# Kernel optimization log

Measured on AMD Instinct MI355X. Metric: run time of the kernel, lower is better.

## Reference

```python
import jax, jax.numpy as jnp
import numpy as np

N = 50000
E = 1_600_000
N_INP = 128
N_HID = 128
N_OUT = 64
N_LAYERS = 2


def setup_inputs() -> dict:
    key = jax.random.key(0)
    ks = jax.random.split(key, 12)
    s = 1.0 / np.sqrt(N_HID)
    return {
        "node_attr": jax.random.normal(ks[0], (N, N_INP), dtype=jnp.float32),
        "edge_index": jax.random.randint(ks[1], (2, E), 0, N, dtype=jnp.int64),
        "batch_idx": jnp.zeros((N,), dtype=jnp.int64),
        "adv_atts": jax.random.uniform(ks[2], (N_LAYERS, E), dtype=jnp.float32, minval=0.05, maxval=1.0),
        "W_inp": jax.random.normal(ks[3], (N_HID, N_INP), dtype=jnp.float32) * (1.0 / np.sqrt(N_INP)),
        "b_inp": jnp.zeros((N_HID,), dtype=jnp.float32),
        "W_a": jax.random.normal(ks[4], (N_LAYERS, N_HID, N_HID), dtype=jnp.float32) * s,
        "b_a": jnp.zeros((N_LAYERS, N_HID), dtype=jnp.float32),
        "ln_w": jnp.ones((N_LAYERS, N_HID), dtype=jnp.float32),
        "ln_b": jnp.zeros((N_LAYERS, N_HID), dtype=jnp.float32),
        "W_out": jax.random.normal(ks[5], (N_OUT, N_HID), dtype=jnp.float32) * s,
        "b_out": jnp.zeros((N_OUT,), dtype=jnp.float32),
    }


def _layer_norm(x, w, b, eps=1e-5):
    mu = jnp.mean(x, axis=-1, keepdims=True)
    var = jnp.mean(jnp.square(x - mu), axis=-1, keepdims=True)
    return (x - mu) * jax.lax.rsqrt(var + eps) * w + b


def _segment_softmax(logits, seg, num_segments):
    # PyG softmax: numerically-stable softmax grouped by target node id
    m = jax.ops.segment_max(logits, seg, num_segments=num_segments)
    e = jnp.exp(logits - m[seg])
    s = jax.ops.segment_sum(e, seg, num_segments=num_segments)
    return e / (s[seg] + 1e-16)


def reference(node_attr, edge_index, batch_idx, adv_atts,
              W_inp, b_inp, W_a, b_a, ln_w, ln_b, W_out, b_out):
    src = edge_index[0]  # j (source)
    dst = edge_index[1]  # i (target)
    n = node_attr.shape[0]
    # dropout is identity at inference; initial norm is overwritten (dead code)
    node_rep = node_attr @ W_inp.T + b_inp  # [N, H]
    for l in range(W_a.shape[0]):
        att = _segment_softmax(jnp.log(adv_atts[l]), dst, n)        # [E]
        msg = node_rep[src] * att[:, None]                          # [E, H]
        aggr = jax.ops.segment_sum(msg, dst, num_segments=n)        # [N, H]
        h = (aggr + node_rep) @ W_a[l].T + b_a[l]
        node_rep = _layer_norm(jax.nn.gelu(h, approximate=False), ln_w[l], ln_b[l])
    # node_level == True
    return node_rep @ W_out.T + b_out
```

## Files before the change

### kernel.cpp

```cpp
#include <hip/hip_runtime.h>
#include <hip/hip_bf16.h>
#include <math.h>


#define WAVE 64
#define NPARTS 32
#define CHUNKE 4096
#define CB 64

typedef __attribute__((ext_vector_type(8))) short bf16x8;
typedef __attribute__((ext_vector_type(4))) float f32x4;
union ABu { uint4 u; bf16x8 v; };
union ABh { ushort h[8]; bf16x8 v; };

static __device__ __forceinline__ float bf2f(uint u16) {
    union { uint i; float f; } c;
    c.i = u16 << 16;
    return c.f;
}
static __device__ __forceinline__ uint f2bf(float f) {
    uint x = __float_as_uint(f);
    return (x + 0x7FFFu + ((x >> 16) & 1u)) >> 16;
}

__global__ void k_count(const int* __restrict__ dst, int E,
                        int* __restrict__ deg, int* __restrict__ rank) {
    int e = blockIdx.x * blockDim.x + threadIdx.x;
    if (e < E) rank[e] = atomicAdd(&deg[dst[e]], 1);
}

__global__ __launch_bounds__(256) void k_scan1(const int* __restrict__ deg, int n,
                                               int* __restrict__ excl,
                                               int* __restrict__ bsum) {
    __shared__ int sd[256];
    int t = threadIdx.x, i = blockIdx.x * 256 + t;
    int v = (i < n) ? deg[i] : 0;
    sd[t] = v;
    __syncthreads();
    for (int off = 1; off < 256; off <<= 1) {
        int u = (t >= off) ? sd[t - off] : 0;
        __syncthreads();
        sd[t] += u;
        __syncthreads();
    }
    if (i < n) excl[i] = sd[t] - v;
    if (t == 255) bsum[blockIdx.x] = sd[255];
}

__global__ __launch_bounds__(256) void k_scan2(int* __restrict__ bsum, int nb) {
    __shared__ int sd[256];
    int t = threadIdx.x;
    int v = (t < nb) ? bsum[t] : 0;
    sd[t] = v;
    __syncthreads();
    for (int off = 1; off < 256; off <<= 1) {
        int u = (t >= off) ? sd[t - off] : 0;
        __syncthreads();
        sd[t] += u;
        __syncthreads();
    }
    if (t < nb) bsum[t] = sd[t] - v;
}

__global__ __launch_bounds__(256) void k_scan3(const int* __restrict__ deg,
                                               const int* __restrict__ excl,
                                               const int* __restrict__ bsum, int n,
                                               int* __restrict__ row_ptr) {
    int i = blockIdx.x * 256 + threadIdx.x;
    if (i < n) {
        int rp = bsum[blockIdx.x] + excl[i];
        row_ptr[i] = rp;
        if (i == n - 1) row_ptr[n] = rp + deg[i];
    }
}

__global__ __launch_bounds__(256) void k_bin(const int* __restrict__ src,
                                             const int* __restrict__ dst,
                                             const float* __restrict__ adv,
                                             const int* __restrict__ rank,
                                             const int* __restrict__ row_ptr,
                                             int E, int PART,
                                             int4* __restrict__ tmp,
                                             int* __restrict__ bstart,
                                             int* __restrict__ bcnt) {
    __shared__ int hist[NPARTS], cur[NPARTS], base_[NPARTS];
    __shared__ int4 buf[CHUNKE];
    int c = blockIdx.x;
    int e0 = c * CHUNKE;
    int cnt = min(CHUNKE, E - e0);
    int dreg[CHUNKE / 256];
    int preg[CHUNKE / 256];
    if (threadIdx.x < NPARTS) hist[threadIdx.x] = 0;
    __syncthreads();
#pragma unroll
    for (int i = 0; i < CHUNKE / 256; ++i) {
        int idx = threadIdx.x + i * 256;
        if (idx < cnt) {
            int d = dst[e0 + idx];
            int pt = d / PART;
            dreg[i] = d;
            preg[i] = pt;
            atomicAdd(&hist[pt], 1);
        }
    }
    __syncthreads();
    if (threadIdx.x == 0) {
        int run = 0;
        for (int p = 0; p < NPARTS; ++p) {
            base_[p] = run;
            cur[p] = run;
            run += hist[p];
        }
    }
    __syncthreads();
#pragma unroll
    for (int i = 0; i < CHUNKE / 256; ++i) {
        int idx = threadIdx.x + i * 256;
        if (idx < cnt) {
            int e = e0 + idx;
            int slot = atomicAdd(&cur[preg[i]], 1);
            int pos = row_ptr[dreg[i]] + rank[e];
            buf[slot] = make_int4(src[e], __float_as_int(adv[e]),
                                  __float_as_int(adv[E + e]), pos);
        }
    }
    __syncthreads();
    for (int i = threadIdx.x; i < cnt; i += 256) tmp[(size_t)e0 + i] = buf[i];
    if (threadIdx.x < NPARTS) {
        bstart[c * NPARTS + threadIdx.x] = e0 + base_[threadIdx.x];
        bcnt[c * NPARTS + threadIdx.x] = hist[threadIdx.x];
    }
}

__global__ __launch_bounds__(256) void k_place(const int4* __restrict__ tmp,
                                               const int* __restrict__ bstart,
                                               const int* __restrict__ bcnt,
                                               int nchunk, int4* __restrict__ csr) {
    int xcd = blockIdx.x & 7;
    int j = blockIdx.x >> 3;
    for (int ph = 0; ph < NPARTS / 8; ++ph) {
        int part = xcd + 8 * ph;
        for (int c = j; c < nchunk; c += CB) {
            int s = bstart[c * NPARTS + part];
            int cnt = bcnt[c * NPARTS + part];
            for (int i = threadIdx.x; i < cnt; i += 256) {
                int4 r = tmp[(size_t)s + i];
                csr[r.w] = r;
            }
        }
    }
}

__global__ __launch_bounds__(512) void k_aggr(const uint* __restrict__ rep32,
                                              const int* __restrict__ row_ptr,
                                              const int4* __restrict__ csr, int aoff,
                                              uint* __restrict__ xout, int n) {
    int wave = threadIdx.x >> 6, lane = threadIdx.x & 63;
    int node = blockIdx.x * 8 + wave;
    if (node >= n) return;
    int s0 = row_ptr[node], s1 = row_ptr[node + 1];
    float accx = 0.f, accy = 0.f, ssum = 0.f, amax = 0.f;
    int s = s0;
    for (; s + 8 <= s1; s += 8) {
        int4 c0 = csr[s], c1 = csr[s + 1], c2 = csr[s + 2], c3 = csr[s + 3];
        int4 c4 = csr[s + 4], c5 = csr[s + 5], c6 = csr[s + 6], c7 = csr[s + 7];
        float a0 = __int_as_float(aoff == 1 ? c0.y : c0.z);
        float a1 = __int_as_float(aoff == 1 ? c1.y : c1.z);
        float a2 = __int_as_float(aoff == 1 ? c2.y : c2.z);
        float a3 = __int_as_float(aoff == 1 ? c3.y : c3.z);
        float a4 = __int_as_float(aoff == 1 ? c4.y : c4.z);
        float a5 = __int_as_float(aoff == 1 ? c5.y : c5.z);
        float a6 = __int_as_float(aoff == 1 ? c6.y : c6.z);
        float a7 = __int_as_float(aoff == 1 ? c7.y : c7.z);
        uint r0 = rep32[(size_t)c0.x * 64 + lane];
        uint r1 = rep32[(size_t)c1.x * 64 + lane];
        uint r2 = rep32[(size_t)c2.x * 64 + lane];
        uint r3 = rep32[(size_t)c3.x * 64 + lane];
        uint r4 = rep32[(size_t)c4.x * 64 + lane];
        uint r5 = rep32[(size_t)c5.x * 64 + lane];
        uint r6 = rep32[(size_t)c6.x * 64 + lane];
        uint r7 = rep32[(size_t)c7.x * 64 + lane];
        ssum += a0 + a1 + a2 + a3 + a4 + a5 + a6 + a7;
        amax = fmaxf(amax, fmaxf(fmaxf(fmaxf(a0, a1), fmaxf(a2, a3)),
                                 fmaxf(fmaxf(a4, a5), fmaxf(a6, a7))));
        accx = fmaf(a0, bf2f(r0 & 0xffffu), accx);
        accy = fmaf(a0, bf2f(r0 >> 16), accy);
        accx = fmaf(a1, bf2f(r1 & 0xffffu), accx);
        accy = fmaf(a1, bf2f(r1 >> 16), accy);
        accx = fmaf(a2, bf2f(r2 & 0xffffu), accx);
        accy = fmaf(a2, bf2f(r2 >> 16), accy);
        accx = fmaf(a3, bf2f(r3 & 0xffffu), accx);
        accy = fmaf(a3, bf2f(r3 >> 16), accy);
        accx = fmaf(a4, bf2f(r4 & 0xffffu), accx);
        accy = fmaf(a4, bf2f(r4 >> 16), accy);
        accx = fmaf(a5, bf2f(r5 & 0xffffu), accx);
        accy = fmaf(a5, bf2f(r5 >> 16), accy);
        accx = fmaf(a6, bf2f(r6 & 0xffffu), accx);
        accy = fmaf(a6, bf2f(r6 >> 16), accy);
        accx = fmaf(a7, bf2f(r7 & 0xffffu), accx);
        accy = fmaf(a7, bf2f(r7 >> 16), accy);
    }
    for (; s < s1; ++s) {
        int4 c = csr[s];
        float a = __int_as_float(aoff == 1 ? c.y : c.z);
        uint r = rep32[(size_t)c.x * 64 + lane];
        ssum += a;
        amax = fmaxf(amax, a);
        accx = fmaf(a, bf2f(r & 0xffffu), accx);
        accy = fmaf(a, bf2f(r >> 16), accy);
    }
    float inv = (s1 > s0) ? 1.f / (ssum + amax * 1e-16f) : 0.f;
    uint m = rep32[(size_t)node * 64 + lane];
    float ox = fmaf(accx, inv, bf2f(m & 0xffffu));
    float oy = fmaf(accy, inv, bf2f(m >> 16));
    xout[(size_t)node * 64 + lane] = f2bf(ox) | (f2bf(oy) << 16);
}

#define WROW 136

__global__ __launch_bounds__(512) void k_mlp(const uint* __restrict__ x32,
                                             const float* __restrict__ W,
                                             const float* __restrict__ b,
                                             const float* __restrict__ lw,
                                             const float* __restrict__ lb,
                                             uint* __restrict__ out32, int n) {
    __shared__ ushort Wbf[128 * WROW];
    uint* wd = (uint*)Wbf;
    for (int idx = threadIdx.x; idx < 128 * 64; idx += 512) {
        int row = idx >> 6, d = idx & 63;
        float2 w2 = *(const float2*)&W[row * 128 + d * 2];
        wd[row * (WROW / 2) + d] = f2bf(w2.x) | (f2bf(w2.y) << 16);
    }
    __syncthreads();
    int wv = threadIdx.x >> 6, l = threadIdx.x & 63;
    int c = l & 15, q = l >> 4;
    int base = blockIdx.x * 256 + wv * 32;
    int r0 = min(base + c, n - 1);
    int r1 = min(base + 16 + c, n - 1);

    f32x4 acc[2][8];
#pragma unroll
    for (int rt = 0; rt < 2; ++rt)
#pragma unroll
        for (int ct = 0; ct < 8; ++ct) acc[rt][ct] = (f32x4){0.f, 0.f, 0.f, 0.f};

#pragma unroll
    for (int kb = 0; kb < 4; ++kb) {
        ABu a0, a1;
        a0.u = *(const uint4*)&x32[(size_t)r0 * 64 + kb * 16 + q * 4];
        a1.u = *(const uint4*)&x32[(size_t)r1 * 64 + kb * 16 + q * 4];
#pragma unroll
        for (int ct = 0; ct < 8; ++ct) {
            bf16x8 bf = *(const bf16x8*)&Wbf[(ct * 16 + c) * WROW + kb * 32 + q * 8];
            acc[0][ct] = __builtin_amdgcn_mfma_f32_16x16x32_bf16(a0.v, bf, acc[0][ct], 0, 0, 0);
            acc[1][ct] = __builtin_amdgcn_mfma_f32_16x16x32_bf16(a1.v, bf, acc[1][ct], 0, 0, 0);
        }
    }

    float bias[8], lwv[8], lbv[8];
#pragma unroll
    for (int ct = 0; ct < 8; ++ct) {
        bias[ct] = b[ct * 16 + c];
        lwv[ct] = lw[ct * 16 + c];
        lbv[ct] = lb[ct * 16 + c];
    }

#pragma unroll
    for (int rt = 0; rt < 2; ++rt) {
#pragma unroll
        for (int ct = 0; ct < 8; ++ct)
#pragma unroll
            for (int i = 0; i < 4; ++i) {
                float h = acc[rt][ct][i] + bias[ct];
                acc[rt][ct][i] = 0.5f * h * (1.f + erff(h * 0.70710678118654752f));
            }
        float mu[4], rstd[4];
#pragma unroll
        for (int i = 0; i < 4; ++i) {
            float s = 0.f;
#pragma unroll
            for (int ct = 0; ct < 8; ++ct) s += acc[rt][ct][i];
            s += __shfl_xor(s, 1);
            s += __shfl_xor(s, 2);
            s += __shfl_xor(s, 4);
            s += __shfl_xor(s, 8);
            mu[i] = s * (1.f / 128.f);
        }
#pragma unroll
        for (int i = 0; i < 4; ++i) {
            float v = 0.f;
#pragma unroll
            for (int ct = 0; ct < 8; ++ct) {
                float d = acc[rt][ct][i] - mu[i];
                v += d * d;
            }
            v += __shfl_xor(v, 1);
            v += __shfl_xor(v, 2);
            v += __shfl_xor(v, 4);
            v += __shfl_xor(v, 8);
            rstd[i] = rsqrtf(v * (1.f / 128.f) + 1e-5f);
        }
#pragma unroll
        for (int ct = 0; ct < 8; ++ct)
#pragma unroll
            for (int i = 0; i < 4; ++i) {
                float o = (acc[rt][ct][i] - mu[i]) * rstd[i] * lwv[ct] + lbv[ct];
                float p = __shfl_xor(o, 1);
                uint dw = (c & 1) ? (f2bf(p) | (f2bf(o) << 16))
                                  : (f2bf(o) | (f2bf(p) << 16));
                int R = base + rt * 16 + q * 4 + i;
                if (R < n && (c & 1) == 0)
                    out32[(size_t)R * 64 + ct * 8 + (c >> 1)] = dw;
            }
    }
}

__global__ __launch_bounds__(512) void k_input(const float* __restrict__ attr,
                                               const float* __restrict__ W,
                                               const float* __restrict__ b,
                                               uint* __restrict__ out32, int n) {
    __shared__ ushort Wbf[128 * WROW];
    uint* wd = (uint*)Wbf;
    for (int idx = threadIdx.x; idx < 128 * 64; idx += 512) {
        int row = idx >> 6, d = idx & 63;
        float2 w2 = *(const float2*)&W[row * 128 + d * 2];
        wd[row * (WROW / 2) + d] = f2bf(w2.x) | (f2bf(w2.y) << 16);
    }
    __syncthreads();
    int wv = threadIdx.x >> 6, l = threadIdx.x & 63;
    int c = l & 15, q = l >> 4;
    int base = blockIdx.x * 256 + wv * 32;
    int r0 = min(base + c, n - 1);
    int r1 = min(base + 16 + c, n - 1);

    f32x4 acc[2][8];
#pragma unroll
    for (int rt = 0; rt < 2; ++rt)
#pragma unroll
        for (int ct = 0; ct < 8; ++ct) acc[rt][ct] = (f32x4){0.f, 0.f, 0.f, 0.f};

#pragma unroll
    for (int kb = 0; kb < 4; ++kb) {
        ABh a0, a1;
        float4 f0 = *(const float4*)&attr[(size_t)r0 * 128 + kb * 32 + q * 8];
        float4 f1 = *(const float4*)&attr[(size_t)r0 * 128 + kb * 32 + q * 8 + 4];
        a0.h[0] = f2bf(f0.x); a0.h[1] = f2bf(f0.y); a0.h[2] = f2bf(f0.z); a0.h[3] = f2bf(f0.w);
        a0.h[4] = f2bf(f1.x); a0.h[5] = f2bf(f1.y); a0.h[6] = f2bf(f1.z); a0.h[7] = f2bf(f1.w);
        float4 g0 = *(const float4*)&attr[(size_t)r1 * 128 + kb * 32 + q * 8];
        float4 g1 = *(const float4*)&attr[(size_t)r1 * 128 + kb * 32 + q * 8 + 4];
        a1.h[0] = f2bf(g0.x); a1.h[1] = f2bf(g0.y); a1.h[2] = f2bf(g0.z); a1.h[3] = f2bf(g0.w);
        a1.h[4] = f2bf(g1.x); a1.h[5] = f2bf(g1.y); a1.h[6] = f2bf(g1.z); a1.h[7] = f2bf(g1.w);
#pragma unroll
        for (int ct = 0; ct < 8; ++ct) {
            bf16x8 bf = *(const bf16x8*)&Wbf[(ct * 16 + c) * WROW + kb * 32 + q * 8];
            acc[0][ct] = __builtin_amdgcn_mfma_f32_16x16x32_bf16(a0.v, bf, acc[0][ct], 0, 0, 0);
            acc[1][ct] = __builtin_amdgcn_mfma_f32_16x16x32_bf16(a1.v, bf, acc[1][ct], 0, 0, 0);
        }
    }
    float bias[8];
#pragma unroll
    for (int ct = 0; ct < 8; ++ct) bias[ct] = b[ct * 16 + c];
#pragma unroll
    for (int rt = 0; rt < 2; ++rt)
#pragma unroll
        for (int ct = 0; ct < 8; ++ct)
#pragma unroll
            for (int i = 0; i < 4; ++i) {
                float o = acc[rt][ct][i] + bias[ct];
                float p = __shfl_xor(o, 1);
                uint dw = (c & 1) ? (f2bf(p) | (f2bf(o) << 16))
                                  : (f2bf(o) | (f2bf(p) << 16));
                int R = base + rt * 16 + q * 4 + i;
                if (R < n && (c & 1) == 0)
                    out32[(size_t)R * 64 + ct * 8 + (c >> 1)] = dw;
            }
}

__global__ __launch_bounds__(512) void k_out(const uint* __restrict__ rep32,
                                             const float* __restrict__ W,
                                             const float* __restrict__ b,
                                             float* __restrict__ out, int n) {
    __shared__ ushort Wbf[64 * WROW];
    uint* wd = (uint*)Wbf;
    for (int idx = threadIdx.x; idx < 64 * 64; idx += 512) {
        int row = idx >> 6, d = idx & 63;
        float2 w2 = *(const float2*)&W[row * 128 + d * 2];
        wd[row * (WROW / 2) + d] = f2bf(w2.x) | (f2bf(w2.y) << 16);
    }
    __syncthreads();
    int wv = threadIdx.x >> 6, l = threadIdx.x & 63;
    int c = l & 15, q = l >> 4;
    int base = blockIdx.x * 256 + wv * 32;
    int r0 = min(base + c, n - 1);
    int r1 = min(base + 16 + c, n - 1);

    f32x4 acc[2][4];
#pragma unroll
    for (int rt = 0; rt < 2; ++rt)
#pragma unroll
        for (int ct = 0; ct < 4; ++ct) acc[rt][ct] = (f32x4){0.f, 0.f, 0.f, 0.f};

#pragma unroll
    for (int kb = 0; kb < 4; ++kb) {
        ABu a0, a1;
        a0.u = *(const uint4*)&rep32[(size_t)r0 * 64 + kb * 16 + q * 4];
        a1.u = *(const uint4*)&rep32[(size_t)r1 * 64 + kb * 16 + q * 4];
#pragma unroll
        for (int ct = 0; ct < 4; ++ct) {
            bf16x8 bf = *(const bf16x8*)&Wbf[(ct * 16 + c) * WROW + kb * 32 + q * 8];
            acc[0][ct] = __builtin_amdgcn_mfma_f32_16x16x32_bf16(a0.v, bf, acc[0][ct], 0, 0, 0);
            acc[1][ct] = __builtin_amdgcn_mfma_f32_16x16x32_bf16(a1.v, bf, acc[1][ct], 0, 0, 0);
        }
    }
    float bias[4];
#pragma unroll
    for (int ct = 0; ct < 4; ++ct) bias[ct] = b[ct * 16 + c];
#pragma unroll
    for (int rt = 0; rt < 2; ++rt)
#pragma unroll
        for (int ct = 0; ct < 4; ++ct)
#pragma unroll
            for (int i = 0; i < 4; ++i) {
                int R = base + rt * 16 + q * 4 + i;
                if (R < n) out[(size_t)R * 64 + ct * 16 + c] = acc[rt][ct][i] + bias[ct];
            }
}

extern "C" void kernel_launch(void* const* d_in, const int* in_sizes, int n_in,
                              void* d_out, int out_size, void* d_ws, size_t ws_size,
                              hipStream_t stream) {
    const float* node_attr = (const float*)d_in[0];
    const int* ei = (const int*)d_in[1];
    const float* adv = (const float*)d_in[3];
    const float* W_inp = (const float*)d_in[4];
    const float* b_inp = (const float*)d_in[5];
    const float* W_a = (const float*)d_in[6];
    const float* b_a = (const float*)d_in[7];
    const float* ln_w = (const float*)d_in[8];
    const float* ln_b = (const float*)d_in[9];
    const float* W_out = (const float*)d_in[10];
    const float* b_out = (const float*)d_in[11];

    const int n = in_sizes[0] / 128;
    const int E = in_sizes[1] / 2;
    const int nchunk = (E + CHUNKE - 1) / CHUNKE;
    const int PART = (n + NPARTS - 1) / NPARTS;

    int4* csr = (int4*)d_ws;
    int4* tmp = csr + E;
    uint* A = (uint*)tmp;
    uint* B = A + (size_t)n * 64;
    int* rank = (int*)(tmp + E);
    int* deg = rank + E;
    int* excl = deg + n;
    int* row_ptr = excl + n;
    int* bsum = row_ptr + n + 1;
    int* bstart = bsum + 256;
    int* bcnt = bstart + (size_t)nchunk * NPARTS;

    const int* src = ei;
    const int* dst = ei + E;

    hipMemsetAsync(deg, 0, (size_t)n * sizeof(int), stream);

    int eb = (E + 255) / 256;
    int nbs = (n + 255) / 256;
    k_count<<<eb, 256, 0, stream>>>(dst, E, deg, rank);
    k_scan1<<<nbs, 256, 0, stream>>>(deg, n, excl, bsum);
    k_scan2<<<1, 256, 0, stream>>>(bsum, nbs);
    k_scan3<<<nbs, 256, 0, stream>>>(deg, excl, bsum, n, row_ptr);
    k_bin<<<nchunk, 256, 0, stream>>>(src, dst, adv, rank, row_ptr, E, PART,
                                      tmp, bstart, bcnt);
    k_place<<<8 * CB, 256, 0, stream>>>(tmp, bstart, bcnt, nchunk, csr);

    int nbd = (n + 255) / 256;
    int nb8 = (n + 7) / 8;
    k_input<<<nbd, 512, 0, stream>>>(node_attr, W_inp, b_inp, A, n);

    k_aggr<<<nb8, 512, 0, stream>>>(A, row_ptr, csr, 1, B, n);
    k_mlp<<<nbd, 512, 0, stream>>>(B, W_a, b_a, ln_w, ln_b, A, n);
    k_aggr<<<nb8, 512, 0, stream>>>(A, row_ptr, csr, 2, B, n);
    k_mlp<<<nbd, 512, 0, stream>>>(B, W_a + 128 * 128, b_a + 128,
                                   ln_w + 128, ln_b + 128, A, n);

    k_out<<<nbd, 512, 0, stream>>>(A, W_out, b_out, (float*)d_out, n);
}
```

Before: 343.8 us.

## Fuse degree counting into binning, merge scans, split CSR per layer

```diff
diff --git a/kernel.cpp b/kernel.cpp
--- a/kernel.cpp
+++ b/kernel.cpp
@@ -23,63 +23,11 @@
     return (x + 0x7FFFu + ((x >> 16) & 1u)) >> 16;
 }
 
-__global__ void k_count(const int* __restrict__ dst, int E,
-                        int* __restrict__ deg, int* __restrict__ rank) {
-    int e = blockIdx.x * blockDim.x + threadIdx.x;
-    if (e < E) rank[e] = atomicAdd(&deg[dst[e]], 1);
-}
-
-__global__ __launch_bounds__(256) void k_scan1(const int* __restrict__ deg, int n,
-                                               int* __restrict__ excl,
-                                               int* __restrict__ bsum) {
-    __shared__ int sd[256];
-    int t = threadIdx.x, i = blockIdx.x * 256 + t;
-    int v = (i < n) ? deg[i] : 0;
-    sd[t] = v;
-    __syncthreads();
-    for (int off = 1; off < 256; off <<= 1) {
-        int u = (t >= off) ? sd[t - off] : 0;
-        __syncthreads();
-        sd[t] += u;
-        __syncthreads();
-    }
-    if (i < n) excl[i] = sd[t] - v;
-    if (t == 255) bsum[blockIdx.x] = sd[255];
-}
-
-__global__ __launch_bounds__(256) void k_scan2(int* __restrict__ bsum, int nb) {
-    __shared__ int sd[256];
-    int t = threadIdx.x;
-    int v = (t < nb) ? bsum[t] : 0;
-    sd[t] = v;
-    __syncthreads();
-    for (int off = 1; off < 256; off <<= 1) {
-        int u = (t >= off) ? sd[t - off] : 0;
-        __syncthreads();
-        sd[t] += u;
-        __syncthreads();
-    }
-    if (t < nb) bsum[t] = sd[t] - v;
-}
-
-__global__ __launch_bounds__(256) void k_scan3(const int* __restrict__ deg,
-                                               const int* __restrict__ excl,
-                                               const int* __restrict__ bsum, int n,
-                                               int* __restrict__ row_ptr) {
-    int i = blockIdx.x * 256 + threadIdx.x;
-    if (i < n) {
-        int rp = bsum[blockIdx.x] + excl[i];
-        row_ptr[i] = rp;
-        if (i == n - 1) row_ptr[n] = rp + deg[i];
-    }
-}
-
 __global__ __launch_bounds__(256) void k_bin(const int* __restrict__ src,
                                              const int* __restrict__ dst,
                                              const float* __restrict__ adv,
-                                             const int* __restrict__ rank,
-                                             const int* __restrict__ row_ptr,
                                              int E, int PART,
+                                             int* __restrict__ deg,
                                              int4* __restrict__ tmp,
                                              int* __restrict__ bstart,
                                              int* __restrict__ bcnt) {
@@ -119,9 +67,10 @@
         if (idx < cnt) {
             int e = e0 + idx;
             int slot = atomicAdd(&cur[preg[i]], 1);
-            int pos = row_ptr[dreg[i]] + rank[e];
+            int rk = atomicAdd(&deg[dreg[i]], 1);
             buf[slot] = make_int4(src[e], __float_as_int(adv[e]),
-                                  __float_as_int(adv[E + e]), pos);
+                                  __float_as_int(adv[E + e]),
+                                  dreg[i] | (rk << 16));
         }
     }
     __syncthreads();
@@ -132,10 +81,56 @@
     }
 }
 
+__global__ __launch_bounds__(256) void k_scan1(const int* __restrict__ deg, int n,
+                                               int* __restrict__ excl,
+                                               int* __restrict__ bsum) {
+    __shared__ int sd[256];
+    int t = threadIdx.x, i = blockIdx.x * 256 + t;
+    int v = (i < n) ? deg[i] : 0;
+    sd[t] = v;
+    __syncthreads();
+    for (int off = 1; off < 256; off <<= 1) {
+        int u = (t >= off) ? sd[t - off] : 0;
+        __syncthreads();
+        sd[t] += u;
+        __syncthreads();
+    }
+    if (i < n) excl[i] = sd[t] - v;
+    if (t == 255) bsum[blockIdx.x] = sd[255];
+}
+
+__global__ __launch_bounds__(256) void k_scan3b(const int* __restrict__ deg,
+                                                const int* __restrict__ excl,
+                                                const int* __restrict__ bsum,
+                                                int nbs, int n,
+                                                int* __restrict__ row_ptr) {
+    __shared__ int sd[256];
+    int t = threadIdx.x;
+    int v = (t < nbs) ? bsum[t] : 0;
+    sd[t] = v;
+    __syncthreads();
+    for (int off = 1; off < 256; off <<= 1) {
+        int u = (t >= off) ? sd[t - off] : 0;
+        __syncthreads();
+        sd[t] += u;
+        __syncthreads();
+    }
+    int pref = (blockIdx.x == 0) ? 0 : sd[blockIdx.x - 1];
+    int i = blockIdx.x * 256 + t;
+    if (i < n) {
+        int rp = pref + excl[i];
+        row_ptr[i] = rp;
+        if (i == n - 1) row_ptr[n] = rp + deg[i];
+    }
+}
+
 __global__ __launch_bounds__(256) void k_place(const int4* __restrict__ tmp,
                                                const int* __restrict__ bstart,
                                                const int* __restrict__ bcnt,
-                                               int nchunk, int4* __restrict__ csr) {
+                                               const int* __restrict__ row_ptr,
+                                               int nchunk,
+                                               int2* __restrict__ csr0,
+                                               int2* __restrict__ csr1) {
     int xcd = blockIdx.x & 7;
     int j = blockIdx.x >> 3;
     for (int ph = 0; ph < NPARTS / 8; ++ph) {
@@ -145,7 +140,11 @@
             int cnt = bcnt[c * NPARTS + part];
             for (int i = threadIdx.x; i < cnt; i += 256) {
                 int4 r = tmp[(size_t)s + i];
-                csr[r.w] = r;
+                int d = r.w & 0xffff;
+                int rk = ((uint)r.w) >> 16;
+                int pos = row_ptr[d] + rk;
+                csr0[pos] = make_int2(r.x, r.y);
+                csr1[pos] = make_int2(r.x, r.z);
             }
         }
     }
@@ -153,7 +152,7 @@
 
 __global__ __launch_bounds__(512) void k_aggr(const uint* __restrict__ rep32,
                                               const int* __restrict__ row_ptr,
-                                              const int4* __restrict__ csr, int aoff,
+                                              const int2* __restrict__ csr,
                                               uint* __restrict__ xout, int n) {
     int wave = threadIdx.x >> 6, lane = threadIdx.x & 63;
     int node = blockIdx.x * 8 + wave;
@@ -162,16 +161,12 @@
     float accx = 0.f, accy = 0.f, ssum = 0.f, amax = 0.f;
     int s = s0;
     for (; s + 8 <= s1; s += 8) {
-        int4 c0 = csr[s], c1 = csr[s + 1], c2 = csr[s + 2], c3 = csr[s + 3];
-        int4 c4 = csr[s + 4], c5 = csr[s + 5], c6 = csr[s + 6], c7 = csr[s + 7];
-        float a0 = __int_as_float(aoff == 1 ? c0.y : c0.z);
-        float a1 = __int_as_float(aoff == 1 ? c1.y : c1.z);
-        float a2 = __int_as_float(aoff == 1 ? c2.y : c2.z);
-        float a3 = __int_as_float(aoff == 1 ? c3.y : c3.z);
-        float a4 = __int_as_float(aoff == 1 ? c4.y : c4.z);
-        float a5 = __int_as_float(aoff == 1 ? c5.y : c5.z);
-        float a6 = __int_as_float(aoff == 1 ? c6.y : c6.z);
-        float a7 = __int_as_float(aoff == 1 ? c7.y : c7.z);
+        int2 c0 = csr[s], c1 = csr[s + 1], c2 = csr[s + 2], c3 = csr[s + 3];
+        int2 c4 = csr[s + 4], c5 = csr[s + 5], c6 = csr[s + 6], c7 = csr[s + 7];
+        float a0 = __int_as_float(c0.y), a1 = __int_as_float(c1.y);
+        float a2 = __int_as_float(c2.y), a3 = __int_as_float(c3.y);
+        float a4 = __int_as_float(c4.y), a5 = __int_as_float(c5.y);
+        float a6 = __int_as_float(c6.y), a7 = __int_as_float(c7.y);
         uint r0 = rep32[(size_t)c0.x * 64 + lane];
         uint r1 = rep32[(size_t)c1.x * 64 + lane];
         uint r2 = rep32[(size_t)c2.x * 64 + lane];
@@ -201,8 +196,8 @@
         accy = fmaf(a7, bf2f(r7 >> 16), accy);
     }
     for (; s < s1; ++s) {
-        int4 c = csr[s];
-        float a = __int_as_float(aoff == 1 ? c.y : c.z);
+        int2 c = csr[s];
+        float a = __int_as_float(c.y);
         uint r = rep32[(size_t)c.x * 64 + lane];
         ssum += a;
         amax = fmaxf(amax, a);
@@ -446,12 +441,12 @@
     const int nchunk = (E + CHUNKE - 1) / CHUNKE;
     const int PART = (n + NPARTS - 1) / NPARTS;
 
-    int4* csr = (int4*)d_ws;
-    int4* tmp = csr + E;
+    int2* csr0 = (int2*)d_ws;
+    int2* csr1 = csr0 + E;
+    int4* tmp = (int4*)(csr1 + E);
     uint* A = (uint*)tmp;
     uint* B = A + (size_t)n * 64;
-    int* rank = (int*)(tmp + E);
-    int* deg = rank + E;
+    int* deg = (int*)(tmp + E);
     int* excl = deg + n;
     int* row_ptr = excl + n;
     int* bsum = row_ptr + n + 1;
@@ -463,23 +458,19 @@
 
     hipMemsetAsync(deg, 0, (size_t)n * sizeof(int), stream);
 
-    int eb = (E + 255) / 256;
     int nbs = (n + 255) / 256;
-    k_count<<<eb, 256, 0, stream>>>(dst, E, deg, rank);
+    k_bin<<<nchunk, 256, 0, stream>>>(src, dst, adv, E, PART, deg, tmp, bstart, bcnt);
     k_scan1<<<nbs, 256, 0, stream>>>(deg, n, excl, bsum);
-    k_scan2<<<1, 256, 0, stream>>>(bsum, nbs);
-    k_scan3<<<nbs, 256, 0, stream>>>(deg, excl, bsum, n, row_ptr);
-    k_bin<<<nchunk, 256, 0, stream>>>(src, dst, adv, rank, row_ptr, E, PART,
-                                      tmp, bstart, bcnt);
-    k_place<<<8 * CB, 256, 0, stream>>>(tmp, bstart, bcnt, nchunk, csr);
+    k_scan3b<<<nbs, 256, 0, stream>>>(deg, excl, bsum, nbs, n, row_ptr);
+    k_place<<<8 * CB, 256, 0, stream>>>(tmp, bstart, bcnt, row_ptr, nchunk, csr0, csr1);
 
     int nbd = (n + 255) / 256;
     int nb8 = (n + 7) / 8;
     k_input<<<nbd, 512, 0, stream>>>(node_attr, W_inp, b_inp, A, n);
 
-    k_aggr<<<nb8, 512, 0, stream>>>(A, row_ptr, csr, 1, B, n);
+    k_aggr<<<nb8, 512, 0, stream>>>(A, row_ptr, csr0, B, n);
     k_mlp<<<nbd, 512, 0, stream>>>(B, W_a, b_a, ln_w, ln_b, A, n);
-    k_aggr<<<nb8, 512, 0, stream>>>(A, row_ptr, csr, 2, B, n);
+    k_aggr<<<nb8, 512, 0, stream>>>(A, row_ptr, csr1, B, n);
     k_mlp<<<nbd, 512, 0, stream>>>(B, W_a + 128 * 128, b_a + 128,
                                    ln_w + 128, ln_b + 128, A, n);
 
```

Measured after the change: 319.2 us. 7.2% less time.
